# Performance work log

Hardware: AMD Instinct MI355X
Metric: run time of the kernel (lower is better)

## Reference

```python
import jax, jax.numpy as jnp
import numpy as np

D_MODEL = 512
D_STATE = 64
D_CONV = 4
EXPAND = 2
D_INNER = EXPAND * D_MODEL  # 1024
DT_RANK = D_MODEL // 16     # 32 (mamba default: ceil(d_model/16))
BATCH = 1
SEQ = 2048


def setup_inputs() -> dict:
    key = jax.random.key(0)
    ks = jax.random.split(key, 10)
    def n(k, shape, scale):
        return jax.random.normal(k, shape, dtype=jnp.float32) * scale
    x = n(ks[0], (BATCH, SEQ, D_MODEL), 1.0)
    ln_g = jnp.ones((D_MODEL,), jnp.float32)
    ln_b = jnp.zeros((D_MODEL,), jnp.float32)
    Win = n(ks[1], (2 * D_INNER, D_MODEL), D_MODEL ** -0.5)
    conv_w = n(ks[2], (D_INNER, 1, D_CONV), 0.5)      # depthwise kernel (O,I/g,K)
    conv_b = n(ks[3], (D_INNER,), 0.02)
    Wx = n(ks[4], (DT_RANK + 2 * D_STATE, D_INNER), D_INNER ** -0.5)
    Wdt = n(ks[5], (D_INNER, DT_RANK), DT_RANK ** -0.5)
    bdt = n(ks[6], (D_INNER,), 0.02)
    # Mamba S4D-real init: A = 1..d_state repeated per channel
    A_log = jnp.log(jnp.tile(jnp.arange(1, D_STATE + 1, dtype=jnp.float32)[None, :], (D_INNER, 1)))
    Dp = jnp.ones((D_INNER,), jnp.float32)
    Wout = n(ks[7], (D_MODEL, D_INNER), D_INNER ** -0.5)
    return dict(x=x, ln_g=ln_g, ln_b=ln_b, Win=Win, conv_w=conv_w, conv_b=conv_b,
                Wx=Wx, Wdt=Wdt, bdt=bdt, A_log=A_log, Dp=Dp, Wout=Wout)


def _layernorm(x, g, b, eps=1e-5):
    mu = jnp.mean(x, axis=-1, keepdims=True)
    xc = x - mu
    var = jnp.mean(xc * xc, axis=-1, keepdims=True)
    return xc * jax.lax.rsqrt(var + eps) * g + b


def _mamba_block(x, ln_g, ln_b, Win, conv_w, conv_b, Wx, Wdt, bdt, A_log, Dp, Wout):
    residual = x
    xn = _layernorm(x, ln_g, ln_b)
    # in_proj -> (x, z) gates
    xz = jnp.einsum('bld,ed->ble', xn, Win)           # (B,L,2*D_INNER)
    xi, z = jnp.split(xz, 2, axis=-1)
    # causal depthwise conv1d (torch pads d_conv-1 both sides then truncates to L == left-pad only)
    xc = jnp.transpose(xi, (0, 2, 1))                 # (B,C,L)
    xc = jax.lax.conv_general_dilated(
        xc, conv_w, window_strides=(1,), padding=[(D_CONV - 1, 0)],
        dimension_numbers=('NCH', 'OIH', 'NCH'), feature_group_count=D_INNER)
    xc = xc + conv_b[None, :, None]
    xi = jax.nn.silu(jnp.transpose(xc, (0, 2, 1)))    # (B,L,D_INNER)
    # x_proj -> dt, B, C
    dbc = jnp.einsum('bld,ed->ble', xi, Wx)           # (B,L,DT_RANK+2N)
    dt = dbc[..., :DT_RANK]
    Bm = dbc[..., DT_RANK:DT_RANK + D_STATE]          # (B,L,N)
    Cm = dbc[..., DT_RANK + D_STATE:]                 # (B,L,N)
    delta = jax.nn.softplus(jnp.einsum('blr,dr->bld', dt, Wdt) + bdt)  # (B,L,D_INNER)
    A = -jnp.exp(A_log)                               # (D_INNER,N), negative
    dA = jnp.exp(delta[..., None] * A)                # (B,L,D_INNER,N) in (0,1)
    dBx = (delta * xi)[..., None] * Bm[:, :, None, :] # (B,L,D_INNER,N)
    def step(h, t):
        dA_t, dBx_t, C_t = t
        h = dA_t * h + dBx_t                          # (B,D_INNER,N)
        y_t = jnp.einsum('bdn,bn->bd', h, C_t)
        return h, y_t
    h0 = jnp.zeros((x.shape[0], D_INNER, D_STATE), x.dtype)
    _, ys = jax.lax.scan(step, h0, (jnp.transpose(dA, (1, 0, 2, 3)),
                                    jnp.transpose(dBx, (1, 0, 2, 3)),
                                    jnp.transpose(Cm, (1, 0, 2))))
    y = jnp.transpose(ys, (1, 0, 2)) + Dp * xi        # skip term D*x
    y = y * jax.nn.silu(z)                            # gate
    out = jnp.einsum('bld,ed->ble', y, Wout)          # out_proj
    return out + residual


def reference(x, ln_g, ln_b, Win, conv_w, conv_b, Wx, Wdt, bdt, A_log, Dp, Wout):
    return _mamba_block(x, ln_g, ln_b, Win, conv_w, conv_b, Wx, Wdt, bdt, A_log, Dp, Wout)
```

## Files before the change

kernel.cpp:

```cpp
#include <hip/hip_runtime.h>
#include <hip/hip_bf16.h>
#include <cstddef>

#define SEQ 2048
#define DM  512
#define DI  1024
#define DR  32
#define DS  64
#define NCHUNK 32
#define CHUNK  64
#define MB (1024 * 1024)
#define NCVT 1696

typedef __attribute__((ext_vector_type(4))) float f32x4;
typedef __attribute__((ext_vector_type(8))) short frag8;

__device__ __forceinline__ unsigned short f2bf(float f) {
    unsigned u = __float_as_uint(f);
    unsigned r = (u + 0x7fffu + ((u >> 16) & 1u)) >> 16;
    return (unsigned short)r;
}
__device__ __forceinline__ float bf2f(unsigned short u) {
    return __int_as_float(((int)u) << 16);
}

__device__ __forceinline__ float fexp2(float x) {
#if __has_builtin(__builtin_amdgcn_exp2f)
    return __builtin_amdgcn_exp2f(x);
#else
    return exp2f(x);
#endif
}
#define LOG2E 1.44269504088896f

template <int CTRL>
__device__ __forceinline__ float dppadd(float p) {
    return p + __int_as_float(
        __builtin_amdgcn_update_dpp(0, __float_as_int(p), CTRL, 0xF, 0xF, true));
}

__global__ void cvt_ln(const float* __restrict__ w1, unsigned short* __restrict__ o1,
                       const float* __restrict__ w2, unsigned short* __restrict__ o2,
                       const float* __restrict__ w3, unsigned short* __restrict__ o3,
                       const float* __restrict__ x, const float* __restrict__ g,
                       const float* __restrict__ b, unsigned short* __restrict__ xn) {
    if (blockIdx.x < NCVT) {
        const int n1 = 1048576, n2 = 163840, n3 = 524288;
        int i = (blockIdx.x * 256 + threadIdx.x) * 4;
        const float* s; unsigned short* d; int off;
        if (i < n1) { s = w1; d = o1; off = i; }
        else if (i < n1 + n2) { s = w2; d = o2; off = i - n1; }
        else if (i < n1 + n2 + n3) { s = w3; d = o3; off = i - n1 - n2; }
        else return;
        float4 v = *(const float4*)(s + off);
        ushort4 o = { f2bf(v.x), f2bf(v.y), f2bf(v.z), f2bf(v.w) };
        *(ushort4*)(d + off) = o;
        return;
    }
    int l = blockIdx.x - NCVT;
    int t = threadIdx.x;
    __shared__ float red[256];
    float v0 = x[l * DM + t];
    float v1 = x[l * DM + t + 256];
    red[t] = v0 + v1;
    __syncthreads();
    for (int o = 128; o > 0; o >>= 1) { if (t < o) red[t] += red[t + o]; __syncthreads(); }
    float mu = red[0] * (1.f / DM);
    __syncthreads();
    float c0 = v0 - mu, c1 = v1 - mu;
    red[t] = c0 * c0 + c1 * c1;
    __syncthreads();
    for (int o = 128; o > 0; o >>= 1) { if (t < o) red[t] += red[t + o]; __syncthreads(); }
    float rstd = rsqrtf(red[0] * (1.f / DM) + 1e-5f);
    xn[l * DM + t]       = f2bf(c0 * rstd * g[t]       + b[t]);
    xn[l * DM + t + 256] = f2bf(c1 * rstd * g[t + 256] + b[t + 256]);
}

#define LDK 40

template <int EPI>
__global__ __launch_bounds__(256, 2)
void gemm_bf(const unsigned short* __restrict__ A, int lda,
             const unsigned short* __restrict__ B, int ldb,
             int N, int K,
             float* __restrict__ outF, const float* __restrict__ res, int ldo,
             float* __restrict__ dtc, unsigned short* __restrict__ bci,
             unsigned short* __restrict__ outB1, unsigned short* __restrict__ outB2) {
    __shared__ unsigned short As[128 * LDK];
    __shared__ unsigned short Bs[64 * LDK];
    int t = threadIdx.x;
    int lane = t & 63;
    int wv = t >> 6;
    int wm = (wv >> 1) * 64;
    int wn = (wv & 1) * 32;
    int m0 = blockIdx.x * 128, n0 = blockIdx.y * 64;

    f32x4 acc[4][2];
#pragma unroll
    for (int i = 0; i < 4; i++)
#pragma unroll
        for (int j = 0; j < 2; j++) acc[i][j] = (f32x4){0.f, 0.f, 0.f, 0.f};

    int lm = lane & 15;
    int kq = (lane >> 4) * 8;

    for (int k0 = 0; k0 < K; k0 += 32) {
#pragma unroll
        for (int j = 0; j < 2; j++) {
            int c = t + j * 256;
            int m = c >> 2;
            int k = (c & 3) * 8;
            frag8 v = *(const frag8*)(A + (size_t)(m0 + m) * lda + k0 + k);
            *(frag8*)(&As[m * LDK + k]) = v;
        }
        {
            int m = t >> 2;
            int k = (t & 3) * 8;
            int gn = n0 + m;
            frag8 v = {0, 0, 0, 0, 0, 0, 0, 0};
            if (gn < N) v = *(const frag8*)(B + (size_t)gn * ldb + k0 + k);
            *(frag8*)(&Bs[m * LDK + k]) = v;
        }
        __syncthreads();

        frag8 af[4], bfr[2];
#pragma unroll
        for (int mt = 0; mt < 4; mt++)
            af[mt] = *(const frag8*)(&As[(wm + mt * 16 + lm) * LDK + kq]);
#pragma unroll
        for (int nt = 0; nt < 2; nt++)
            bfr[nt] = *(const frag8*)(&Bs[(wn + nt * 16 + lm) * LDK + kq]);
#pragma unroll
        for (int mt = 0; mt < 4; mt++)
#pragma unroll
            for (int nt = 0; nt < 2; nt++)
                acc[mt][nt] = __builtin_amdgcn_mfma_f32_16x16x32_bf16(
                    af[mt], bfr[nt], acc[mt][nt], 0, 0, 0);
        __syncthreads();
    }

    int rbase = (lane >> 4) * 4;
#pragma unroll
    for (int mt = 0; mt < 4; mt++) {
#pragma unroll
        for (int nt = 0; nt < 2; nt++) {
            int n = n0 + wn + nt * 16 + lm;
            int mb = m0 + wm + mt * 16 + rbase;
            if (EPI == 1) {
                if (n < DI) {
#pragma unroll
                    for (int r = 0; r < 4; r++)
                        outB1[(size_t)(mb + r) * DI + n] = f2bf(acc[mt][nt][r]);
                } else {
                    int nn = n - DI;
                    ushort4 o;
#pragma unroll
                    for (int r = 0; r < 4; r++) {
                        float v = acc[mt][nt][r];
                        v = v / (1.f + __expf(-v));
                        (&o.x)[r] = f2bf(v);
                    }
                    *(ushort4*)(outB2 + (size_t)nn * SEQ + mb) = o;
                }
            } else if (EPI == 2) {
                if (n < N) {
#pragma unroll
                    for (int r = 0; r < 4; r++)
                        outF[(size_t)(mb + r) * ldo + n] =
                            acc[mt][nt][r] + res[(size_t)(mb + r) * ldo + n];
                }
            } else {
                if (n < 32) {
#pragma unroll
                    for (int r = 0; r < 4; r++)
                        dtc[(size_t)(mb + r) * 32 + n] = acc[mt][nt][r];
                } else if (n < 96) {
                    int col = 2 * (n - 32);
#pragma unroll
                    for (int r = 0; r < 4; r++)
                        bci[(size_t)(mb + r) * 128 + col] = f2bf(acc[mt][nt][r]);
                } else if (n < 160) {
                    int col = 2 * (n - 96) + 1;
#pragma unroll
                    for (int r = 0; r < 4; r++)
                        bci[(size_t)(mb + r) * 128 + col] = f2bf(acc[mt][nt][r]);
                }
            }
        }
    }
}

__global__ void gemm_dt_t(const float* __restrict__ A,
                          const float* __restrict__ B,
                          const float* __restrict__ bias,
                          float* __restrict__ outT) {
    __shared__ float As[16][65];
    __shared__ float Bs[16][65];
    int tid = threadIdx.x;
    int tx = tid & 15, ty = tid >> 4;
    int bm = blockIdx.x * 64, bn = blockIdx.y * 64;
    float acc[4][4] = {};
    int kk = tid & 15;
    int rr = tid >> 4;
    for (int k0 = 0; k0 < DR; k0 += 16) {
#pragma unroll
        for (int i = 0; i < 4; i++)
            As[kk][rr + 16 * i] = A[(size_t)(bm + rr + 16 * i) * 32 + k0 + kk];
#pragma unroll
        for (int i = 0; i < 4; i++)
            Bs[kk][rr + 16 * i] = B[(size_t)(bn + rr + 16 * i) * DR + k0 + kk];
        __syncthreads();
#pragma unroll
        for (int k = 0; k < 16; k++) {
            float a[4], bb[4];
#pragma unroll
            for (int i = 0; i < 4; i++) a[i] = As[k][ty * 4 + i];
#pragma unroll
            for (int j = 0; j < 4; j++) bb[j] = Bs[k][tx * 4 + j];
#pragma unroll
            for (int i = 0; i < 4; i++)
#pragma unroll
                for (int j = 0; j < 4; j++)
                    acc[i][j] = fmaf(a[i], bb[j], acc[i][j]);
        }
        __syncthreads();
    }
#pragma unroll
    for (int j = 0; j < 4; j++) {
        int e = bn + tx * 4 + j;
        float bv = bias[e];
        float4 o;
#pragma unroll
        for (int i = 0; i < 4; i++) {
            float v = acc[i][j] + bv;
            v = (v > 20.f) ? v : __logf(1.f + __expf(v));
            (&o.x)[i] = v;
        }
        *(float4*)(outT + (size_t)e * SEQ + bm + ty * 4) = o;
    }
}

__global__ void conv_t(const unsigned short* __restrict__ xi_raw,
                       const float* __restrict__ w, const float* __restrict__ cb,
                       unsigned short* __restrict__ xi2bf, unsigned short* __restrict__ xi2T) {
    __shared__ float tin[67][72];
    __shared__ float tout[64][65];
    int l0 = blockIdx.x * 64, e0 = blockIdx.y * 64;
    int t = threadIdx.x;
    for (int c = t; c < 536; c += 256) {
        int r = c >> 3, ke = (c & 7) * 8;
        int l = l0 - 3 + r;
        frag8 v = {0, 0, 0, 0, 0, 0, 0, 0};
        if (l >= 0) v = *(const frag8*)(xi_raw + (size_t)l * DI + e0 + ke);
#pragma unroll
        for (int i = 0; i < 8; i++) tin[r][ke + i] = bf2f((unsigned short)v[i]);
    }
    __syncthreads();
    int e_loc = t & 63;
    int e = e0 + e_loc;
    float4 wv = *(const float4*)(w + e * 4);
    float bias = cb[e];
#pragma unroll 4
    for (int i = 0; i < 16; i++) {
        int l_loc = (t >> 6) + i * 4;
        float acc = bias;
        acc = fmaf(wv.x, tin[l_loc][e_loc], acc);
        acc = fmaf(wv.y, tin[l_loc + 1][e_loc], acc);
        acc = fmaf(wv.z, tin[l_loc + 2][e_loc], acc);
        acc = fmaf(wv.w, tin[l_loc + 3][e_loc], acc);
        float s = acc / (1.f + __expf(-acc));
        tout[l_loc][e_loc] = s;
        xi2bf[(size_t)(l0 + l_loc) * DI + e] = f2bf(s);
    }
    __syncthreads();
    for (int c = t; c < 1024; c += 256) {
        int er = c >> 4, l4 = (c & 15) * 4;
        ushort4 o = { f2bf(tout[l4][er]), f2bf(tout[l4 + 1][er]),
                      f2bf(tout[l4 + 2][er]), f2bf(tout[l4 + 3][er]) };
        *(ushort4*)(xi2T + (size_t)(e0 + er) * SEQ + l0 + l4) = o;
    }
}

__global__ void scan_passA(const float* __restrict__ deltaT, const unsigned short* __restrict__ xi2T,
                           const unsigned short* __restrict__ bci, const float* __restrict__ A_log,
                           float* __restrict__ sumd, float* __restrict__ hend) {
    int wid = blockIdx.x * 4 + (threadIdx.x >> 6);
    int eg = wid & 255;
    int c  = wid >> 8;
    int lane = threadIdx.x & 63;
    int g = lane >> 4;
    int i = lane & 15;
    int e = eg * 4 + g;
    int l0 = c * CHUNK;
    float4 al = *(const float4*)(A_log + e * DS + 4 * i);
    float Ae2[4];
#pragma unroll
    for (int k = 0; k < 4; k++) Ae2[k] = -__expf((&al.x)[k]) * LOG2E;
    float h[4] = {0.f, 0.f, 0.f, 0.f};
    float sum_d = 0.f;
    const float4* d4  = (const float4*)(deltaT + (size_t)e * SEQ + l0);
    const ushort4* x4 = (const ushort4*)(xi2T + (size_t)e * SEQ + l0);
    const uint4* bc4  = (const uint4*)((const unsigned*)bci + (size_t)l0 * 64) + i;
    for (int gq = 0; gq < CHUNK / 4; gq++) {
        float4 dd = d4[gq];
        ushort4 xx = x4[gq];
#pragma unroll
        for (int j = 0; j < 4; j++) {
            uint4 bcv = bc4[(4 * gq + j) * 16];
            float dj = (&dd.x)[j];
            float dx = dj * bf2f((&xx.x)[j]);
            sum_d += dj;
#pragma unroll
            for (int k = 0; k < 4; k++) {
                float dA = fexp2(dj * Ae2[k]);
                float Bk = __int_as_float((&bcv.x)[k] << 16);
                h[k] = fmaf(dA, h[k], dx * Bk);
            }
        }
    }
    size_t idx = ((size_t)c * DI + e) * DS + 4 * i;
    float4 hv = {h[0], h[1], h[2], h[3]};
    *(float4*)(hend + idx) = hv;
    if (i == 0) sumd[c * DI + e] = sum_d;
}

__global__ void scan_carry(float* __restrict__ hend, const float* __restrict__ sumd,
                           const float* __restrict__ A_log) {
    int e = blockIdx.x * 4 + (threadIdx.x >> 6);
    int n = threadIdx.x & 63;
    float Ae2 = -__expf(A_log[e * DS + n]) * LOG2E;
    float h = 0.f;
    for (int c = 0; c < NCHUNK; c++) {
        size_t idx = ((size_t)c * DI + e) * DS + n;
        if (c < NCHUNK - 1) {
            float he = hend[idx];
            float P = fexp2(Ae2 * sumd[c * DI + e]);
            hend[idx] = h;
            h = fmaf(P, h, he);
        } else {
            hend[idx] = h;
        }
    }
}

__global__ void scan_passB(const float* __restrict__ deltaT, const unsigned short* __restrict__ xi2T,
                           const unsigned short* __restrict__ bci, const unsigned short* __restrict__ szT,
                           const float* __restrict__ A_log, const float* __restrict__ Dp,
                           const float* __restrict__ hin, unsigned short* __restrict__ y_bf) {
    int wid = blockIdx.x * 4 + (threadIdx.x >> 6);
    int eg = wid & 255;
    int c  = wid >> 8;
    int lane = threadIdx.x & 63;
    int g = lane >> 4;
    int i = lane & 15;
    int e = eg * 4 + g;
    int l0 = c * CHUNK;
    float4 al = *(const float4*)(A_log + e * DS + 4 * i);
    float Ae2[4];
#pragma unroll
    for (int k = 0; k < 4; k++) Ae2[k] = -__expf((&al.x)[k]) * LOG2E;
    float dp = Dp[e];
    float4 hv = *(const float4*)(hin + ((size_t)c * DI + e) * DS + 4 * i);
    float h[4] = {hv.x, hv.y, hv.z, hv.w};
    const float4* d4  = (const float4*)(deltaT + (size_t)e * SEQ + l0);
    const ushort4* x4 = (const ushort4*)(xi2T + (size_t)e * SEQ + l0);
    const ushort4* s4 = (const ushort4*)(szT + (size_t)e * SEQ + l0);
    const uint4* bc4  = (const uint4*)((const unsigned*)bci + (size_t)l0 * 64) + i;
    for (int gq = 0; gq < CHUNK / 4; gq++) {
        float4 dd = d4[gq];
        ushort4 xx = x4[gq], zz = s4[gq];
        ushort4 yv;
#pragma unroll
        for (int j = 0; j < 4; j++) {
            uint4 bcv = bc4[(4 * gq + j) * 16];
            float dj = (&dd.x)[j];
            float xj = bf2f((&xx.x)[j]);
            float dx = dj * xj;
            float Ck[4];
#pragma unroll
            for (int k = 0; k < 4; k++) {
                unsigned w = (&bcv.x)[k];
                float Bk = __int_as_float(w << 16);
                Ck[k] = __int_as_float(w & 0xffff0000u);
                float dA = fexp2(dj * Ae2[k]);
                h[k] = fmaf(dA, h[k], dx * Bk);
            }
            float p = h[0] * Ck[0];
            p = fmaf(h[1], Ck[1], p);
            p = fmaf(h[2], Ck[2], p);
            p = fmaf(h[3], Ck[3], p);
            p = dppadd<0xB1>(p);
            p = dppadd<0x4E>(p);
            p = dppadd<0x141>(p);
            p = dppadd<0x140>(p);
            (&yv.x)[j] = f2bf((p + dp * xj) * bf2f((&zz.x)[j]));
        }
        if (i == 0) {
#pragma unroll
            for (int j = 0; j < 4; j++)
                y_bf[(size_t)(l0 + 4 * gq + j) * DI + e] = (&yv.x)[j];
        }
    }
}

extern "C" void kernel_launch(void* const* d_in, const int* in_sizes, int n_in,
                              void* d_out, int out_size, void* d_ws, size_t ws_size,
                              hipStream_t stream) {
    const float* x      = (const float*)d_in[0];
    const float* ln_g   = (const float*)d_in[1];
    const float* ln_b   = (const float*)d_in[2];
    const float* Win    = (const float*)d_in[3];
    const float* conv_w = (const float*)d_in[4];
    const float* conv_b = (const float*)d_in[5];
    const float* Wx     = (const float*)d_in[6];
    const float* Wdt    = (const float*)d_in[7];
    const float* bdt    = (const float*)d_in[8];
    const float* A_log  = (const float*)d_in[9];
    const float* Dp     = (const float*)d_in[10];
    const float* Wout   = (const float*)d_in[11];
    float* out = (float*)d_out;

    char* W = (char*)d_ws;
    unsigned short* xi_raw  = (unsigned short*)W;
    float*          deltaT  = (float*)W;
    unsigned short* Win_bf  = (unsigned short*)(W + 8 * MB);
    unsigned short* xi2bf   = (unsigned short*)(W + 8 * MB);
    unsigned short* y_bf    = (unsigned short*)(W + 8 * MB);
    unsigned short* szT     = (unsigned short*)(W + 12 * MB);
    unsigned short* xi2T    = (unsigned short*)(W + 16 * MB);
    unsigned short* xn_bf   = (unsigned short*)(W + 20 * MB);
    float*          hend    = (float*)(W + 20 * MB);
    unsigned short* Wout_bf = (unsigned short*)(W + 28 * MB);
    float*          sumd    = (float*)(W + 29 * MB);
    unsigned short* Wx_bf   = (unsigned short*)(W + 29 * MB + 128 * 1024);
    float*          dtc     = (float*)(W + 29 * MB + 448 * 1024);
    unsigned short* bci     = (unsigned short*)(W + 29 * MB + 704 * 1024);

    cvt_ln<<<NCVT + SEQ, 256, 0, stream>>>(Win, Win_bf, Wx, Wx_bf, Wout, Wout_bf,
                                           x, ln_g, ln_b, xn_bf);

    gemm_bf<1><<<dim3(SEQ / 128, 2048 / 64), 256, 0, stream>>>(
        xn_bf, DM, Win_bf, DM, 2048, DM, nullptr, nullptr, 0, nullptr, nullptr,
        xi_raw, szT);

    conv_t<<<dim3(SEQ / 64, DI / 64), 256, 0, stream>>>(xi_raw, conv_w, conv_b, xi2bf, xi2T);

    gemm_bf<4><<<dim3(SEQ / 128, 3), 256, 0, stream>>>(
        xi2bf, DI, Wx_bf, DI, 160, DI, nullptr, nullptr, 0, dtc, bci, nullptr, nullptr);

    gemm_dt_t<<<dim3(SEQ / 64, DI / 64), 256, 0, stream>>>(dtc, Wdt, bdt, deltaT);

    scan_passA<<<(DI / 4) * (NCHUNK - 1) / 4, 256, 0, stream>>>(deltaT, xi2T, bci, A_log, sumd, hend);
    scan_carry<<<DI / 4, 256, 0, stream>>>(hend, sumd, A_log);
    scan_passB<<<(DI / 4) * NCHUNK / 4, 256, 0, stream>>>(deltaT, xi2T, bci, szT,
                                                          A_log, Dp, hend, y_bf);

    gemm_bf<2><<<dim3(SEQ / 128, DM / 64), 256, 0, stream>>>(
        y_bf, DI, Wout_bf, DI, DM, DI, out, x, DM, nullptr, nullptr, nullptr, nullptr);
}
```

Baseline: 235.4 us.

## Fold dt_proj weights into x_proj GEMM and preload carry-scan inputs

Precomputes the product Wdt·Wx[:32] as a bf16 1024x1024 weight block and stacks it under the B/C rows of Wx. A single bf16 MFMA GEMM then produces B, C and softplus(delta) directly (N=1152), which removes the separate fp32 dt GEMM kernel and the dtc intermediate. This adds a weight-fusion kernel on every call, makes the x_proj GEMM much larger (K=1024 for 1024 extra columns), and rounds the fused weight to bf16, which changes numerics. The carry-scan kernel is also changed to load all chunk values into registers before running its serial recurrence.

Result: no change. 236.9 us (+0.6%).

```diff
diff --git a/kernel.cpp b/kernel.cpp
--- a/kernel.cpp
+++ b/kernel.cpp
@@ -10,7 +10,7 @@
 #define NCHUNK 32
 #define CHUNK  64
 #define MB (1024 * 1024)
-#define NCVT 1696
+#define NCVT 1664
 
 typedef __attribute__((ext_vector_type(4))) float f32x4;
 typedef __attribute__((ext_vector_type(8))) short frag8;
@@ -39,13 +39,52 @@
         __builtin_amdgcn_update_dpp(0, __float_as_int(p), CTRL, 0xF, 0xF, true));
 }
 
+__global__ void wfused_kernel(const float* __restrict__ Wdt, const float* __restrict__ Wx,
+                              unsigned short* __restrict__ WxBC) {
+    __shared__ float As[DR][65];
+    __shared__ float Bs[DR][65];
+    int t = threadIdx.x;
+    int e0 = blockIdx.x * 64, k0 = blockIdx.y * 64;
+    for (int c = t; c < 512; c += 256) {
+        int er = c >> 3, r4 = (c & 7) * 4;
+        float4 v = *(const float4*)(Wdt + (size_t)(e0 + er) * DR + r4);
+        As[r4][er] = v.x; As[r4 + 1][er] = v.y; As[r4 + 2][er] = v.z; As[r4 + 3][er] = v.w;
+    }
+    for (int c = t; c < 512; c += 256) {
+        int rr = c >> 4, k4 = (c & 15) * 4;
+        float4 v = *(const float4*)(Wx + (size_t)rr * DI + k0 + k4);
+        Bs[rr][k4] = v.x; Bs[rr][k4 + 1] = v.y; Bs[rr][k4 + 2] = v.z; Bs[rr][k4 + 3] = v.w;
+    }
+    __syncthreads();
+    int tx = t & 15, ty = t >> 4;
+    float acc[4][4] = {};
+#pragma unroll
+    for (int r = 0; r < DR; r++) {
+        float a[4], b[4];
+#pragma unroll
+        for (int i = 0; i < 4; i++) a[i] = As[r][ty * 4 + i];
+#pragma unroll
+        for (int j = 0; j < 4; j++) b[j] = Bs[r][tx * 4 + j];
+#pragma unroll
+        for (int i = 0; i < 4; i++)
+#pragma unroll
+            for (int j = 0; j < 4; j++)
+                acc[i][j] = fmaf(a[i], b[j], acc[i][j]);
+    }
+#pragma unroll
+    for (int i = 0; i < 4; i++) {
+        ushort4 o = { f2bf(acc[i][0]), f2bf(acc[i][1]), f2bf(acc[i][2]), f2bf(acc[i][3]) };
+        *(ushort4*)(WxBC + (size_t)(128 + e0 + ty * 4 + i) * DI + k0 + tx * 4) = o;
+    }
+}
+
 __global__ void cvt_ln(const float* __restrict__ w1, unsigned short* __restrict__ o1,
                        const float* __restrict__ w2, unsigned short* __restrict__ o2,
                        const float* __restrict__ w3, unsigned short* __restrict__ o3,
                        const float* __restrict__ x, const float* __restrict__ g,
                        const float* __restrict__ b, unsigned short* __restrict__ xn) {
     if (blockIdx.x < NCVT) {
-        const int n1 = 1048576, n2 = 163840, n3 = 524288;
+        const int n1 = 1048576, n2 = 131072, n3 = 524288;
         int i = (blockIdx.x * 256 + threadIdx.x) * 4;
         const float* s; unsigned short* d; int off;
         if (i < n1) { s = w1; d = o1; off = i; }
@@ -84,7 +123,7 @@
              const unsigned short* __restrict__ B, int ldb,
              int N, int K,
              float* __restrict__ outF, const float* __restrict__ res, int ldo,
-             float* __restrict__ dtc, unsigned short* __restrict__ bci,
+             unsigned short* __restrict__ bci,
              unsigned short* __restrict__ outB1, unsigned short* __restrict__ outB2) {
     __shared__ unsigned short As[128 * LDK];
     __shared__ unsigned short Bs[64 * LDK];
@@ -170,73 +209,30 @@
                             acc[mt][nt][r] + res[(size_t)(mb + r) * ldo + n];
                 }
             } else {
-                if (n < 32) {
-#pragma unroll
-                    for (int r = 0; r < 4; r++)
-                        dtc[(size_t)(mb + r) * 32 + n] = acc[mt][nt][r];
-                } else if (n < 96) {
-                    int col = 2 * (n - 32);
+                if (n < 64) {
+                    int col = 2 * n;
 #pragma unroll
                     for (int r = 0; r < 4; r++)
                         bci[(size_t)(mb + r) * 128 + col] = f2bf(acc[mt][nt][r]);
-                } else if (n < 160) {
-                    int col = 2 * (n - 96) + 1;
+                } else if (n < 128) {
+                    int col = 2 * (n - 64) + 1;
 #pragma unroll
                     for (int r = 0; r < 4; r++)
                         bci[(size_t)(mb + r) * 128 + col] = f2bf(acc[mt][nt][r]);
+                } else {
+                    int e = n - 128;
+                    float bv = res[e];
+                    float4 o;
+#pragma unroll
+                    for (int r = 0; r < 4; r++) {
+                        float v = acc[mt][nt][r] + bv;
+                        v = (v > 20.f) ? v : __logf(1.f + __expf(v));
+                        (&o.x)[r] = v;
+                    }
+                    *(float4*)(outF + (size_t)e * SEQ + mb) = o;
                 }
             }
         }
-    }
-}
-
-__global__ void gemm_dt_t(const float* __restrict__ A,
-                          const float* __restrict__ B,
-                          const float* __restrict__ bias,
-                          float* __restrict__ outT) {
-    __shared__ float As[16][65];
-    __shared__ float Bs[16][65];
-    int tid = threadIdx.x;
-    int tx = tid & 15, ty = tid >> 4;
-    int bm = blockIdx.x * 64, bn = blockIdx.y * 64;
-    float acc[4][4] = {};
-    int kk = tid & 15;
-    int rr = tid >> 4;
-    for (int k0 = 0; k0 < DR; k0 += 16) {
-#pragma unroll
-        for (int i = 0; i < 4; i++)
-            As[kk][rr + 16 * i] = A[(size_t)(bm + rr + 16 * i) * 32 + k0 + kk];
-#pragma unroll
-        for (int i = 0; i < 4; i++)
-            Bs[kk][rr + 16 * i] = B[(size_t)(bn + rr + 16 * i) * DR + k0 + kk];
-        __syncthreads();
-#pragma unroll
-        for (int k = 0; k < 16; k++) {
-            float a[4], bb[4];
-#pragma unroll
-            for (int i = 0; i < 4; i++) a[i] = As[k][ty * 4 + i];
-#pragma unroll
-            for (int j = 0; j < 4; j++) bb[j] = Bs[k][tx * 4 + j];
-#pragma unroll
-            for (int i = 0; i < 4; i++)
-#pragma unroll
-                for (int j = 0; j < 4; j++)
-                    acc[i][j] = fmaf(a[i], bb[j], acc[i][j]);
-        }
-        __syncthreads();
-    }
-#pragma unroll
-    for (int j = 0; j < 4; j++) {
-        int e = bn + tx * 4 + j;
-        float bv = bias[e];
-        float4 o;
-#pragma unroll
-        for (int i = 0; i < 4; i++) {
-            float v = acc[i][j] + bv;
-            v = (v > 20.f) ? v : __logf(1.f + __expf(v));
-            (&o.x)[i] = v;
-        }
-        *(float4*)(outT + (size_t)e * SEQ + bm + ty * 4) = o;
     }
 }
 
@@ -329,18 +325,21 @@
     int e = blockIdx.x * 4 + (threadIdx.x >> 6);
     int n = threadIdx.x & 63;
     float Ae2 = -__expf(A_log[e * DS + n]) * LOG2E;
+    float he[NCHUNK - 1], sd[NCHUNK - 1];
+#pragma unroll
+    for (int c = 0; c < NCHUNK - 1; c++)
+        he[c] = hend[((size_t)c * DI + e) * DS + n];
+#pragma unroll
+    for (int c = 0; c < NCHUNK - 1; c++)
+        sd[c] = sumd[c * DI + e];
     float h = 0.f;
-    for (int c = 0; c < NCHUNK; c++) {
-        size_t idx = ((size_t)c * DI + e) * DS + n;
-        if (c < NCHUNK - 1) {
-            float he = hend[idx];
-            float P = fexp2(Ae2 * sumd[c * DI + e]);
-            hend[idx] = h;
-            h = fmaf(P, h, he);
-        } else {
-            hend[idx] = h;
-        }
-    }
+#pragma unroll
+    for (int c = 0; c < NCHUNK - 1; c++) {
+        float P = fexp2(Ae2 * sd[c]);
+        hend[((size_t)c * DI + e) * DS + n] = h;
+        h = fmaf(P, h, he[c]);
+    }
+    hend[((size_t)(NCHUNK - 1) * DI + e) * DS + n] = h;
 }
 
 __global__ void scan_passB(const float* __restrict__ deltaT, const unsigned short* __restrict__ xi2T,
@@ -429,26 +428,25 @@
     unsigned short* szT     = (unsigned short*)(W + 12 * MB);
     unsigned short* xi2T    = (unsigned short*)(W + 16 * MB);
     unsigned short* xn_bf   = (unsigned short*)(W + 20 * MB);
+    unsigned short* WxBC    = (unsigned short*)(W + 22 * MB);
     float*          hend    = (float*)(W + 20 * MB);
     unsigned short* Wout_bf = (unsigned short*)(W + 28 * MB);
     float*          sumd    = (float*)(W + 29 * MB);
-    unsigned short* Wx_bf   = (unsigned short*)(W + 29 * MB + 128 * 1024);
-    float*          dtc     = (float*)(W + 29 * MB + 448 * 1024);
-    unsigned short* bci     = (unsigned short*)(W + 29 * MB + 704 * 1024);
-
-    cvt_ln<<<NCVT + SEQ, 256, 0, stream>>>(Win, Win_bf, Wx, Wx_bf, Wout, Wout_bf,
-                                           x, ln_g, ln_b, xn_bf);
+    unsigned short* bci     = (unsigned short*)(W + 29 * MB + 128 * 1024);
+
+    wfused_kernel<<<dim3(DI / 64, DI / 64), 256, 0, stream>>>(Wdt, Wx, WxBC);
+
+    cvt_ln<<<NCVT + SEQ, 256, 0, stream>>>(Win, Win_bf, Wx + 32 * DI, WxBC,
+                                           Wout, Wout_bf, x, ln_g, ln_b, xn_bf);
 
     gemm_bf<1><<<dim3(SEQ / 128, 2048 / 64), 256, 0, stream>>>(
-        xn_bf, DM, Win_bf, DM, 2048, DM, nullptr, nullptr, 0, nullptr, nullptr,
+        xn_bf, DM, Win_bf, DM, 2048, DM, nullptr, nullptr, 0, nullptr,
         xi_raw, szT);
 
     conv_t<<<dim3(SEQ / 64, DI / 64), 256, 0, stream>>>(xi_raw, conv_w, conv_b, xi2bf, xi2T);
 
-    gemm_bf<4><<<dim3(SEQ / 128, 3), 256, 0, stream>>>(
-        xi2bf, DI, Wx_bf, DI, 160, DI, nullptr, nullptr, 0, dtc, bci, nullptr, nullptr);
-
-    gemm_dt_t<<<dim3(SEQ / 64, DI / 64), 256, 0, stream>>>(dtc, Wdt, bdt, deltaT);
+    gemm_bf<5><<<dim3(SEQ / 128, 1152 / 64), 256, 0, stream>>>(
+        xi2bf, DI, WxBC, DI, 1152, DI, deltaT, bdt, 0, bci, nullptr, nullptr);
 
     scan_passA<<<(DI / 4) * (NCHUNK - 1) / 4, 256, 0, stream>>>(deltaT, xi2T, bci, A_log, sumd, hend);
     scan_carry<<<DI / 4, 256, 0, stream>>>(hend, sumd, A_log);
@@ -456,5 +454,5 @@
                                                           A_log, Dp, hend, y_bf);
 
     gemm_bf<2><<<dim3(SEQ / 128, DM / 64), 256, 0, stream>>>(
-        y_bf, DI, Wout_bf, DI, DM, DI, out, x, DM, nullptr, nullptr, nullptr, nullptr);
-}
+        y_bf, DI, Wout_bf, DI, DM, DI, out, x, DM, nullptr, nullptr, nullptr);
+}
```
